# Kernel tuning notes

Measured on AMD Instinct MI355X. Metric: run time of the kernel, lower is better.

## Reference

```python
import jax, jax.numpy as jnp
import numpy as np

B, L, Q, H = 8192, 200, 128, 128

def setup_inputs() -> dict:
    key = jax.random.key(0)
    k1, k2, k3, k4 = jax.random.split(key, 4)
    query_ad = jax.random.normal(k1, (B, Q), dtype=jnp.float32)
    hist_behavior = jax.random.normal(k2, (B, L, H), dtype=jnp.float32)
    hist_behavior_length = jax.random.randint(k3, (B,), 0, L, dtype=jnp.int64)
    # xavier_normal for [Q, H] weight: std = sqrt(2/(Q+H))
    std = float(np.sqrt(2.0 / (Q + H)))
    biInt_weight = jax.random.normal(k4, (Q, H), dtype=jnp.float32) * std
    return {
        "query_ad": query_ad,
        "hist_behavior": hist_behavior,
        "hist_behavior_length": hist_behavior_length,
        "biInt_weight": biInt_weight,
    }

def reference(query_ad, hist_behavior, hist_behavior_length, biInt_weight):
    # bilinear attention logits: [B, L]
    logits = jnp.einsum('bq,qh,blh->bl', query_ad, biInt_weight, hist_behavior)
    # faithful to original: mask fills positions where arange < length with 1e-9
    L_ = hist_behavior.shape[1]
    mask = jnp.arange(L_)[None, :] < hist_behavior_length[:, None]  # [B, L]
    logits = jnp.where(mask, jnp.float32(1e-9), logits)
    score = jax.nn.softmax(logits, axis=-1)  # [B, L]
    out = jnp.einsum('bl,blh->bh', score, hist_behavior)  # [B, H]
    return out
```

## Files before the change

kernel.cpp:

```cpp
#include <hip/hip_runtime.h>
#include <math.h>

#define L_SEQ 200
#define Q_DIM 128
#define H_DIM 128

__global__ __launch_bounds__(256, 3) void attn_pool(
    const float* __restrict__ query,
    const float* __restrict__ hist,
    const int*   __restrict__ lens,
    const float* __restrict__ W,
    float* __restrict__ out)
{
    const int b = blockIdx.x;
    const int t = threadIdx.x;
    const int lane32 = t & 31;
    const int lgroup = t >> 5;
    const int wid    = t >> 6;

    __shared__ float s_q[Q_DIM];
    __shared__ float s_qw[H_DIM];
    __shared__ float s_part[8 * H_DIM];
    __shared__ float s_logits[L_SEQ];
    __shared__ float s_red[4];
    __shared__ float s_scalar[2];

    if (t < Q_DIM) s_q[t] = query[(size_t)b * Q_DIM + t];
    __syncthreads();
    {
        const int h  = t & 127;
        const int qh = t >> 7;
        float acc = 0.f;
        #pragma unroll 8
        for (int i = 0; i < 64; ++i) {
            const int q = qh * 64 + i;
            acc = fmaf(s_q[q], W[q * H_DIM + h], acc);
        }
        s_part[t] = acc;
    }
    __syncthreads();
    if (t < H_DIM) s_qw[t] = s_part[t] + s_part[t + 128];
    __syncthreads();

    const float4 qw4 = reinterpret_cast<const float4*>(s_qw)[lane32];

    const float* hrow = hist + (size_t)b * (L_SEQ * H_DIM);
    float4 r[25];
    #pragma unroll
    for (int i = 0; i < 25; ++i) {
        const int l = i * 8 + lgroup;
        r[i] = reinterpret_cast<const float4*>(hrow + l * H_DIM)[lane32];
    }

    #pragma unroll
    for (int i = 0; i < 25; ++i) {
        float p = qw4.x * r[i].x + qw4.y * r[i].y + qw4.z * r[i].z + qw4.w * r[i].w;
        p += __shfl_down(p, 16, 32);
        p += __shfl_down(p, 8, 32);
        p += __shfl_down(p, 4, 32);
        p += __shfl_down(p, 2, 32);
        p += __shfl_down(p, 1, 32);
        if (lane32 == 0) s_logits[i * 8 + lgroup] = p;
    }
    __syncthreads();

    const int len = lens[b];
    float x = -3.0e38f;
    if (t < L_SEQ) {
        const float v = s_logits[t];
        x = (t < len) ? 1e-9f : v;
    }
    float m = x;
    m = fmaxf(m, __shfl_down(m, 32));
    m = fmaxf(m, __shfl_down(m, 16));
    m = fmaxf(m, __shfl_down(m, 8));
    m = fmaxf(m, __shfl_down(m, 4));
    m = fmaxf(m, __shfl_down(m, 2));
    m = fmaxf(m, __shfl_down(m, 1));
    if ((t & 63) == 0) s_red[wid] = m;
    __syncthreads();
    if (t == 0)
        s_scalar[0] = fmaxf(fmaxf(s_red[0], s_red[1]), fmaxf(s_red[2], s_red[3]));
    __syncthreads();
    const float gmax = s_scalar[0];

    float e = 0.f;
    if (t < L_SEQ) {
        e = __expf(x - gmax);
        s_logits[t] = e;
    }
    float ssum = e;
    ssum += __shfl_down(ssum, 32);
    ssum += __shfl_down(ssum, 16);
    ssum += __shfl_down(ssum, 8);
    ssum += __shfl_down(ssum, 4);
    ssum += __shfl_down(ssum, 2);
    ssum += __shfl_down(ssum, 1);
    if ((t & 63) == 0) s_red[wid] = ssum;
    __syncthreads();
    if (t == 0) s_scalar[1] = s_red[0] + s_red[1] + s_red[2] + s_red[3];
    __syncthreads();
    const float inv = 1.0f / s_scalar[1];

    float4 acc = make_float4(0.f, 0.f, 0.f, 0.f);
    #pragma unroll
    for (int i = 0; i < 25; ++i) {
        const float s = s_logits[i * 8 + lgroup] * inv;
        acc.x = fmaf(s, r[i].x, acc.x);
        acc.y = fmaf(s, r[i].y, acc.y);
        acc.z = fmaf(s, r[i].z, acc.z);
        acc.w = fmaf(s, r[i].w, acc.w);
    }
    reinterpret_cast<float4*>(s_part)[lgroup * 32 + lane32] = acc;
    __syncthreads();
    if (t < H_DIM) {
        float v = 0.f;
        #pragma unroll
        for (int g = 0; g < 8; ++g) v += s_part[g * H_DIM + t];
        out[(size_t)b * H_DIM + t] = v;
    }
}

extern "C" void kernel_launch(void* const* d_in, const int* in_sizes, int n_in,
                              void* d_out, int out_size, void* d_ws, size_t ws_size,
                              hipStream_t stream) {
    const float* query = (const float*)d_in[0];
    const float* hist  = (const float*)d_in[1];
    const int*   lens  = (const int*)d_in[2];
    const float* W     = (const float*)d_in[3];
    float* out = (float*)d_out;

    const int B = in_sizes[2];
    attn_pool<<<dim3(B), dim3(256), 0, stream>>>(query, hist, lens, W, out);
}
```

Baseline: 1.037 ms.

## Split query-weight projection into its own kernel and widen pooling blocks to 512 threads

```diff
diff --git a/kernel.cpp b/kernel.cpp
--- a/kernel.cpp
+++ b/kernel.cpp
@@ -5,11 +5,27 @@
 #define Q_DIM 128
 #define H_DIM 128
 
-__global__ __launch_bounds__(256, 3) void attn_pool(
+__global__ __launch_bounds__(128) void qw_kernel(
     const float* __restrict__ query,
+    const float* __restrict__ W,
+    float* __restrict__ qw)
+{
+    const int b = blockIdx.x;
+    const int h = threadIdx.x;
+    __shared__ float s_q[Q_DIM];
+    s_q[h] = query[(size_t)b * Q_DIM + h];
+    __syncthreads();
+    float acc = 0.f;
+    #pragma unroll 8
+    for (int q = 0; q < Q_DIM; ++q)
+        acc = fmaf(s_q[q], W[q * H_DIM + h], acc);
+    qw[(size_t)b * H_DIM + h] = acc;
+}
+
+__global__ __launch_bounds__(512, 4) void attn_pool(
+    const float* __restrict__ qw,
     const float* __restrict__ hist,
     const int*   __restrict__ lens,
-    const float* __restrict__ W,
     float* __restrict__ out)
 {
     const int b = blockIdx.x;
@@ -18,49 +34,41 @@
     const int lgroup = t >> 5;
     const int wid    = t >> 6;
 
-    __shared__ float s_q[Q_DIM];
-    __shared__ float s_qw[H_DIM];
-    __shared__ float s_part[8 * H_DIM];
     __shared__ float s_logits[L_SEQ];
-    __shared__ float s_red[4];
+    __shared__ float s_part[16 * H_DIM];
+    __shared__ float s_red[8];
     __shared__ float s_scalar[2];
 
-    if (t < Q_DIM) s_q[t] = query[(size_t)b * Q_DIM + t];
-    __syncthreads();
-    {
-        const int h  = t & 127;
-        const int qh = t >> 7;
-        float acc = 0.f;
-        #pragma unroll 8
-        for (int i = 0; i < 64; ++i) {
-            const int q = qh * 64 + i;
-            acc = fmaf(s_q[q], W[q * H_DIM + h], acc);
-        }
-        s_part[t] = acc;
-    }
-    __syncthreads();
-    if (t < H_DIM) s_qw[t] = s_part[t] + s_part[t + 128];
-    __syncthreads();
-
-    const float4 qw4 = reinterpret_cast<const float4*>(s_qw)[lane32];
+    const float4 qw4 =
+        reinterpret_cast<const float4*>(qw + (size_t)b * H_DIM)[lane32];
 
     const float* hrow = hist + (size_t)b * (L_SEQ * H_DIM);
-    float4 r[25];
+    const bool tail = (lgroup < 8);
+    float4 r[13];
     #pragma unroll
-    for (int i = 0; i < 25; ++i) {
-        const int l = i * 8 + lgroup;
-        r[i] = reinterpret_cast<const float4*>(hrow + l * H_DIM)[lane32];
-    }
+    for (int i = 0; i < 12; ++i)
+        r[i] = reinterpret_cast<const float4*>(hrow + (i * 16 + lgroup) * H_DIM)[lane32];
+    if (tail)
+        r[12] = reinterpret_cast<const float4*>(hrow + (192 + lgroup) * H_DIM)[lane32];
 
     #pragma unroll
-    for (int i = 0; i < 25; ++i) {
+    for (int i = 0; i < 12; ++i) {
         float p = qw4.x * r[i].x + qw4.y * r[i].y + qw4.z * r[i].z + qw4.w * r[i].w;
         p += __shfl_down(p, 16, 32);
         p += __shfl_down(p, 8, 32);
         p += __shfl_down(p, 4, 32);
         p += __shfl_down(p, 2, 32);
         p += __shfl_down(p, 1, 32);
-        if (lane32 == 0) s_logits[i * 8 + lgroup] = p;
+        if (lane32 == 0) s_logits[i * 16 + lgroup] = p;
+    }
+    if (tail) {
+        float p = qw4.x * r[12].x + qw4.y * r[12].y + qw4.z * r[12].z + qw4.w * r[12].w;
+        p += __shfl_down(p, 16, 32);
+        p += __shfl_down(p, 8, 32);
+        p += __shfl_down(p, 4, 32);
+        p += __shfl_down(p, 2, 32);
+        p += __shfl_down(p, 1, 32);
+        if (lane32 == 0) s_logits[192 + lgroup] = p;
     }
     __syncthreads();
 
@@ -79,8 +87,12 @@
     m = fmaxf(m, __shfl_down(m, 1));
     if ((t & 63) == 0) s_red[wid] = m;
     __syncthreads();
-    if (t == 0)
-        s_scalar[0] = fmaxf(fmaxf(s_red[0], s_red[1]), fmaxf(s_red[2], s_red[3]));
+    if (t == 0) {
+        float g = s_red[0];
+        #pragma unroll
+        for (int i = 1; i < 8; ++i) g = fmaxf(g, s_red[i]);
+        s_scalar[0] = g;
+    }
     __syncthreads();
     const float gmax = s_scalar[0];
 
@@ -98,25 +110,37 @@
     ssum += __shfl_down(ssum, 1);
     if ((t & 63) == 0) s_red[wid] = ssum;
     __syncthreads();
-    if (t == 0) s_scalar[1] = s_red[0] + s_red[1] + s_red[2] + s_red[3];
+    if (t == 0) {
+        float g = 0.f;
+        #pragma unroll
+        for (int i = 0; i < 8; ++i) g += s_red[i];
+        s_scalar[1] = g;
+    }
     __syncthreads();
     const float inv = 1.0f / s_scalar[1];
 
     float4 acc = make_float4(0.f, 0.f, 0.f, 0.f);
     #pragma unroll
-    for (int i = 0; i < 25; ++i) {
-        const float s = s_logits[i * 8 + lgroup] * inv;
+    for (int i = 0; i < 12; ++i) {
+        const float s = s_logits[i * 16 + lgroup] * inv;
         acc.x = fmaf(s, r[i].x, acc.x);
         acc.y = fmaf(s, r[i].y, acc.y);
         acc.z = fmaf(s, r[i].z, acc.z);
         acc.w = fmaf(s, r[i].w, acc.w);
+    }
+    if (tail) {
+        const float s = s_logits[192 + lgroup] * inv;
+        acc.x = fmaf(s, r[12].x, acc.x);
+        acc.y = fmaf(s, r[12].y, acc.y);
+        acc.z = fmaf(s, r[12].z, acc.z);
+        acc.w = fmaf(s, r[12].w, acc.w);
     }
     reinterpret_cast<float4*>(s_part)[lgroup * 32 + lane32] = acc;
     __syncthreads();
     if (t < H_DIM) {
         float v = 0.f;
         #pragma unroll
-        for (int g = 0; g < 8; ++g) v += s_part[g * H_DIM + t];
+        for (int g = 0; g < 16; ++g) v += s_part[g * H_DIM + t];
         out[(size_t)b * H_DIM + t] = v;
     }
 }
@@ -129,7 +153,9 @@
     const int*   lens  = (const int*)d_in[2];
     const float* W     = (const float*)d_in[3];
     float* out = (float*)d_out;
+    float* qw  = (float*)d_ws;
 
     const int B = in_sizes[2];
-    attn_pool<<<dim3(B), dim3(256), 0, stream>>>(query, hist, lens, W, out);
+    qw_kernel<<<dim3(B), dim3(128), 0, stream>>>(query, W, qw);
+    attn_pool<<<dim3(B), dim3(512), 0, stream>>>(qw, hist, lens, out);
 }
```

Result: no change. 1.055 ms (+1.8%).
